# Kernel optimization log

Hardware: AMD Instinct MI355X
Metric: run time of the kernel (lower is better)

The kernel has to match this reference:

```python
import jax, jax.numpy as jnp
import numpy as np

B, L, K = 4, 1024, 48
EF, NF, NPE, NRBF, NCLS = 128, 128, 16, 16, 3
MAXREL = 32
EDGE_IN = NPE + NRBF * 25  # 416


def setup_inputs():
    key = jax.random.key(0)
    ks = jax.random.split(key, 8)
    X = jax.random.normal(ks[0], (B, L, 4, 3), jnp.float32)
    mask = jnp.ones((B, L), jnp.float32)
    R_idx = jnp.arange(B * L, dtype=jnp.int64).reshape(B, L)
    chain_labels = jax.random.randint(ks[1], (B, L), 0, 4).astype(jnp.int64)
    membrane_per_residue_labels = jax.random.randint(ks[2], (B, L), 0, NCLS).astype(jnp.int64)
    pe_w = jax.random.normal(ks[3], (2 * MAXREL + 2, NPE), jnp.float32) * 0.05
    pe_b = jax.random.normal(ks[4], (NPE,), jnp.float32) * 0.05
    edge_w = jax.random.normal(ks[5], (EDGE_IN, EF), jnp.float32) * 0.05
    ne_g = jnp.ones((EF,), jnp.float32)
    ne_b = jnp.zeros((EF,), jnp.float32)
    node_w = jax.random.normal(ks[6], (NCLS, NF), jnp.float32) * 0.05
    nn_g = jnp.ones((NF,), jnp.float32)
    nn_b = jnp.zeros((NF,), jnp.float32)
    return {"X": X, "mask": mask, "R_idx": R_idx, "chain_labels": chain_labels,
            "membrane_per_residue_labels": membrane_per_residue_labels,
            "pe_w": pe_w, "pe_b": pe_b, "edge_w": edge_w, "ne_g": ne_g, "ne_b": ne_b,
            "node_w": node_w, "nn_g": nn_g, "nn_b": nn_b}


def _rbf(D):
    mu = jnp.linspace(2.0, 22.0, NRBF)
    sigma = (22.0 - 2.0) / NRBF
    return jnp.exp(-(((D[..., None] - mu) / sigma) ** 2))


def _gather_nb(v, e_idx):
    # v: [B, L, ...] -> [B, L, K, ...] gathered along residue dim
    return jax.vmap(lambda vi, ii: vi[ii])(v, e_idx)


def _ln(x, g, b, eps=1e-5):
    mu = jnp.mean(x, -1, keepdims=True)
    var = jnp.mean((x - mu) ** 2, -1, keepdims=True)
    return (x - mu) / jnp.sqrt(var + eps) * g + b


# 24 atom-pair RBFs after the Ca-Ca (D_neighbors) one, in the original concat order
PAIRS = [("N","N"),("C","C"),("O","O"),("Cb","Cb"),("Ca","N"),("Ca","C"),("Ca","O"),
         ("Ca","Cb"),("N","C"),("N","O"),("N","Cb"),("Cb","C"),("Cb","O"),("O","C"),
         ("N","Ca"),("C","Ca"),("O","Ca"),("Cb","Ca"),("C","N"),("O","N"),("Cb","N"),
         ("C","Cb"),("O","Cb"),("C","O")]


def reference(X, mask, R_idx, chain_labels, membrane_per_residue_labels,
              pe_w, pe_b, edge_w, ne_g, ne_b, node_w, nn_g, nn_b):
    Na, Ca, Cc, Oo = X[:, :, 0], X[:, :, 1], X[:, :, 2], X[:, :, 3]
    bvec = Ca - Na
    cvec = Cc - Ca
    avec = jnp.cross(bvec, cvec)
    Cb = -0.58273431 * avec + 0.56802827 * bvec - 0.54067466 * cvec + Ca
    coords = {"N": Na, "Ca": Ca, "C": Cc, "O": Oo, "Cb": Cb}

    # masked Ca-Ca distances + kNN (single NxN pass)
    mask2 = mask[:, :, None] * mask[:, None, :]
    dX = Ca[:, :, None, :] - Ca[:, None, :, :]
    D = mask2 * jnp.sqrt(jnp.sum(dX ** 2, -1) + 1e-6)
    D_max = jnp.max(D, -1, keepdims=True)
    D_adj = D + (1.0 - mask2) * D_max
    negD, E_idx = jax.lax.top_k(-D_adj, K)
    D_neighbors = -negD  # [B, L, K]

    # gather neighbor coords once, compute the 25 RBF features on N*K pairs only
    nb = {n: _gather_nb(v, E_idx) for n, v in coords.items()}  # [B, L, K, 3]
    rbf_list = [_rbf(D_neighbors)]
    for an, bn in PAIRS:
        d = jnp.sqrt(jnp.sum((coords[an][:, :, None, :] - nb[bn]) ** 2, -1) + 1e-6)
        rbf_list.append(_rbf(d))
    RBF_all = jnp.concatenate(rbf_list, -1)  # [B, L, K, 400]

    # positional encodings on gathered offsets / chain equality
    off = R_idx[:, :, None] - _gather_nb(R_idx, E_idx)           # [B, L, K]
    E_chains = (chain_labels[:, :, None] == _gather_nb(chain_labels, E_idx)).astype(jnp.int32)
    d = jnp.clip(off + MAXREL, 0, 2 * MAXREL).astype(jnp.int32) * E_chains + (1 - E_chains) * (2 * MAXREL + 1)
    d1h = jax.nn.one_hot(d, 2 * MAXREL + 2, dtype=jnp.float32)
    E_pos = d1h @ pe_w + pe_b                                     # [B, L, K, 16]

    E = jnp.concatenate([E_pos, RBF_all], -1) @ edge_w            # [B, L, K, 128]
    E = _ln(E, ne_g, ne_b)

    C1h = jax.nn.one_hot(membrane_per_residue_labels, NCLS, dtype=jnp.float32)
    V = _ln(C1h @ node_w, nn_g, nn_b)                             # [B, L, 128]
    return V, E, E_idx
```

## Files before the change

kernel.cpp:

```cpp
#include <hip/hip_runtime.h>
#include <math.h>

#define B_ 4
#define L_ 1024
#define K_ 48
#define EF_ 128
#define NF_ 128
#define NPE_ 16
#define NRBF_ 16
#define MAXREL_ 32
#define EDGE_IN_ 416

#define V_SIZE   (B_*L_*NF_)
#define E_OFF    (V_SIZE)
#define E_SIZE   (B_*L_*K_*EF_)
#define EIDX_OFF (E_OFF + E_SIZE)

#define XH_STRIDE 232

typedef __attribute__((ext_vector_type(8))) short bf16x8;
typedef __attribute__((ext_vector_type(4))) float f32x4;
typedef __attribute__((ext_vector_type(4))) unsigned u32x4;

__device__ const int PA_[25] = {1, 0,2,3,4, 1,1,1,1, 0,0,0, 4,4, 3, 0,2,3,4, 2,3,4, 2,3, 2};
__device__ const int PB_[25] = {1, 0,2,3,4, 0,2,3,4, 2,3,4, 2,3, 2, 1,1,1,1, 0,0,0, 4,4, 3};

__device__ __forceinline__ unsigned short f2bf(float f){
    unsigned u = __float_as_uint(f);
    unsigned r = u + 0x7fffu + ((u >> 16) & 1u);
    return (unsigned short)(r >> 16);
}

__device__ __forceinline__ float pair_dist(const float* sAI, const float (*sAJ)[16], int e, int g2) {
    float dx = sAI[PA_[g2]*3+0] - sAJ[e][PB_[g2]*3+0];
    float dy = sAI[PA_[g2]*3+1] - sAJ[e][PB_[g2]*3+1];
    float dz = sAI[PA_[g2]*3+2] - sAJ[e][PB_[g2]*3+2];
    return sqrtf(dx*dx + dy*dy + dz*dz + 1e-6f);
}

__device__ __forceinline__ void rbf16(unsigned short* dst, float dist) {
    float t = 0.8f * dist - 1.6f;
    unsigned pk[8];
    #pragma unroll
    for (int rr = 0; rr < 8; ++rr) {
        float v0 = __expf(-t * t); t -= 1.06666672f;
        float v1 = __expf(-t * t); t -= 1.06666672f;
        asm("v_cvt_pk_bf16_f32 %0, %1, %2" : "=v"(pk[rr]) : "v"(v0), "v"(v1));
    }
    u32x4 w0 = {pk[0], pk[1], pk[2], pk[3]};
    u32x4 w1 = {pk[4], pk[5], pk[6], pk[7]};
    *(u32x4*)dst = w0;
    *(u32x4*)(dst + 8) = w1;
}

template<int NKS, int KB>
__device__ __forceinline__ void mfma_half(f32x4 (&acc)[3][2], const unsigned short* xh,
                                          const unsigned short* w0p, const unsigned short* w1p,
                                          int lr, int lg) {
    #pragma unroll
    for (int ks = 0; ks < NKS; ++ks) {
        int k0 = ks * 32;
        bf16x8 a0, a1, a2, wb0, wb1;
        wb0 = *(const bf16x8*)(w0p + KB + k0);
        wb1 = *(const bf16x8*)(w1p + KB + k0);
        a0 = *(const bf16x8*)&xh[(lr)      * XH_STRIDE + k0 + lg*8];
        a1 = *(const bf16x8*)&xh[(16 + lr) * XH_STRIDE + k0 + lg*8];
        a2 = *(const bf16x8*)&xh[(32 + lr) * XH_STRIDE + k0 + lg*8];
        acc[0][0] = __builtin_amdgcn_mfma_f32_16x16x32_bf16(a0, wb0, acc[0][0], 0, 0, 0);
        acc[0][1] = __builtin_amdgcn_mfma_f32_16x16x32_bf16(a0, wb1, acc[0][1], 0, 0, 0);
        acc[1][0] = __builtin_amdgcn_mfma_f32_16x16x32_bf16(a1, wb0, acc[1][0], 0, 0, 0);
        acc[1][1] = __builtin_amdgcn_mfma_f32_16x16x32_bf16(a1, wb1, acc[1][1], 0, 0, 0);
        acc[2][0] = __builtin_amdgcn_mfma_f32_16x16x32_bf16(a2, wb0, acc[2][0], 0, 0, 0);
        acc[2][1] = __builtin_amdgcn_mfma_f32_16x16x32_bf16(a2, wb1, acc[2][1], 0, 0, 0);
    }
}

__global__ __launch_bounds__(256) void wprep_kernel(const float* __restrict__ w,
                                                    unsigned short* __restrict__ wt)
{
    int idx = blockIdx.x * 256 + threadIdx.x;
    if (idx >= EDGE_IN_ * EF_) return;
    int f = idx & 127;
    int k = idx >> 7;
    wt[f * EDGE_IN_ + k] = f2bf(w[k * EF_ + f]);
}

__global__ __launch_bounds__(128) void v_kernel(const int* __restrict__ labels,
                                                const float* __restrict__ node_w,
                                                const float* __restrict__ g,
                                                const float* __restrict__ bb,
                                                float* __restrict__ out)
{
    int gi = blockIdx.x;
    int f  = threadIdx.x;
    int lbl = labels[gi];
    float v = node_w[lbl*NF_ + f];

    __shared__ float red[2];
    __shared__ float red2[2];
    float s = v;
    #pragma unroll
    for (int m = 1; m < 64; m <<= 1) s += __shfl_xor(s, m, 64);
    if ((f & 63) == 0) red[f >> 6] = s;
    __syncthreads();
    float mu = (red[0] + red[1]) * (1.0f / NF_);
    float d = v - mu;
    float s2 = d * d;
    #pragma unroll
    for (int m = 1; m < 64; m <<= 1) s2 += __shfl_xor(s2, m, 64);
    if ((f & 63) == 0) red2[f >> 6] = s2;
    __syncthreads();
    float var = (red2[0] + red2[1]) * (1.0f / NF_);
    out[gi*NF_ + f] = d * rsqrtf(var + 1e-5f) * g[f] + bb[f];
}

__global__ __launch_bounds__(256, 6) void fused_kernel(const float* __restrict__ X,
                                                   const float* __restrict__ mask,
                                                   const int* __restrict__ Ridx,
                                                   const int* __restrict__ chains,
                                                   const float* __restrict__ pe_w,
                                                   const float* __restrict__ pe_b,
                                                   const unsigned short* __restrict__ wt,
                                                   const float* __restrict__ ne_g,
                                                   const float* __restrict__ ne_b,
                                                   float* __restrict__ out)
{
    __shared__ __align__(16) unsigned char sBuf[K_ * XH_STRIDE * 2];
    __shared__ float sAI[16];
    __shared__ float sAJ[K_][16];
    __shared__ int   sJ[K_];
    __shared__ int   sDpos[K_];
    __shared__ float wmax[4];
    __shared__ unsigned wsum[4];
    __shared__ int sSelBin;
    __shared__ unsigned sSelLo, sSelCnt, sCnt, sCnt2;
    __shared__ unsigned long long sTkey;

    unsigned* hist32 = (unsigned*)sBuf;
    unsigned short* xh = (unsigned short*)sBuf;
    unsigned long long* cand = (unsigned long long*)(sBuf + 16384);
    float* stats  = (float*)(sBuf + 16384);
    float* stats2 = (float*)(sBuf + 17152);

    int tid = threadIdx.x;
    int gi  = blockIdx.x;
    int b   = gi >> 10;
    int i   = gi & (L_ - 1);

    const float* Xb = X + ((size_t)(b << 10)) * 12;
    const float* mb = mask + (b << 10);
    float cx, cy, cz, mi;
    {
        const float* xi = Xb + (size_t)i * 12 + 3;
        cx = xi[0]; cy = xi[1]; cz = xi[2];
        mi = mb[i];
    }
    if (tid == 0) { sCnt = 0; sCnt2 = 0; }

    float dist4[4], m2r[4];
    float lmax = 0.0f;
    #pragma unroll
    for (int q = 0; q < 4; ++q) {
        int j = tid + q * 256;
        const float* xj = Xb + (size_t)j * 12 + 3;
        float dx = cx - xj[0];
        float dy = cy - xj[1];
        float dz = cz - xj[2];
        float dist = sqrtf(dx*dx + dy*dy + dz*dz + 1e-6f);
        float m2 = mi * mb[j];
        dist4[q] = dist; m2r[q] = m2;
        lmax = fmaxf(lmax, m2 * dist);
    }
    #pragma unroll
    for (int m = 1; m < 64; m <<= 1) lmax = fmaxf(lmax, __shfl_xor(lmax, m, 64));
    if ((tid & 63) == 0) wmax[tid >> 6] = lmax;
    __syncthreads();
    float Dmax = fmaxf(fmaxf(wmax[0], wmax[1]), fmaxf(wmax[2], wmax[3]));

    unsigned long long key[4];
    #pragma unroll
    for (int q = 0; q < 4; ++q) {
        int j = tid + q * 256;
        float Dadj = m2r[q] * dist4[q] + (1.0f - m2r[q]) * Dmax;
        key[q] = (((unsigned long long)__float_as_uint(Dadj)) << 32) | (unsigned)j;
    }

    for (int k = tid; k < 4096; k += 256) hist32[k] = 0;
    __syncthreads();
    #pragma unroll
    for (int q = 0; q < 4; ++q)
        atomicAdd(&hist32[(unsigned)(key[q] >> 51) & 0xFFFu], 1u);
    __syncthreads();

    u32x4 h4[4];
    #pragma unroll
    for (int k = 0; k < 4; ++k) h4[k] = *(u32x4*)&hist32[tid*16 + k*4];
    unsigned loc[16], tot = 0;
    #pragma unroll
    for (int k = 0; k < 16; ++k) { tot += h4[k>>2][k&3]; loc[k] = tot; }
    unsigned ws = tot;
    #pragma unroll
    for (int m = 1; m < 64; m <<= 1) {
        unsigned o = __shfl_up(ws, m, 64);
        if ((tid & 63) >= m) ws += o;
    }
    if ((tid & 63) == 63) wsum[tid >> 6] = ws;
    __syncthreads();
    unsigned base = ws - tot;
    for (int w = 0; w < (tid >> 6); ++w) base += wsum[w];
    unsigned lo_t = base;
    #pragma unroll
    for (int k = 0; k < 16; ++k) {
        unsigned hi_t = base + loc[k];
        if (47u >= lo_t && 47u < hi_t) { sSelBin = tid*16 + k; sSelLo = lo_t; sSelCnt = hi_t - lo_t; }
        lo_t = hi_t;
    }
    __syncthreads();
    unsigned bsel = (unsigned)sSelBin, lo = sSelLo, c = sSelCnt;
    unsigned long long T;

    if (c == 1) {
        #pragma unroll
        for (int q = 0; q < 4; ++q)
            if (((unsigned)(key[q] >> 51) & 0xFFFu) == bsel) sTkey = key[q];
        __syncthreads();
        T = sTkey;
    } else if (c <= 64) {
        #pragma unroll
        for (int q = 0; q < 4; ++q)
            if (((unsigned)(key[q] >> 51) & 0xFFFu) == bsel) {
                unsigned pos = atomicAdd(&sCnt, 1u);
                cand[pos] = key[q];
            }
        __syncthreads();
        if (tid < 64) {
            unsigned long long k64 = (tid < (int)c) ? cand[tid] : 0xffffffffffffffffULL;
            #pragma unroll
            for (unsigned kk = 2; kk <= 64; kk <<= 1) {
                #pragma unroll
                for (unsigned jj = kk >> 1; jj > 0; jj >>= 1) {
                    unsigned long long o = __shfl_xor(k64, jj, 64);
                    bool lower = (tid & jj) == 0;
                    bool asc   = (tid & kk) == 0;
                    unsigned long long mn = (k64 < o) ? k64 : o;
                    unsigned long long mx = (k64 < o) ? o : k64;
                    k64 = (lower == asc) ? mn : mx;
                }
            }
            if (tid == (int)(47u - lo)) sTkey = k64;
        }
        __syncthreads();
        T = sTkey;
    } else {
        bool act[4] = {true, true, true, true};
        unsigned r = K_ - 1;
        T = 0;
        const int shifts[6] = {56, 48, 40, 32, 8, 0};
        #pragma unroll 1
        for (int p = 0; p < 6; ++p) {
            int sh = shifts[p];
            hist32[tid] = 0;
            __syncthreads();
            #pragma unroll
            for (int q = 0; q < 4; ++q)
                if (act[q]) atomicAdd(&hist32[(unsigned)((key[q] >> sh) & 255ULL)], 1u);
            __syncthreads();
            if (tid < 64) {
                unsigned b0 = hist32[tid*4+0], b1 = hist32[tid*4+1], b2 = hist32[tid*4+2], b3 = hist32[tid*4+3];
                unsigned s0 = b0, s1 = s0 + b1, s2 = s1 + b2, s3 = s2 + b3;
                unsigned s = s3;
                #pragma unroll
                for (int m = 1; m < 64; m <<= 1) {
                    unsigned o = __shfl_up(s, m, 64);
                    if (tid >= m) s += o;
                }
                unsigned bse = s - s3;
                hist32[tid*4+0] = bse + s0;
                hist32[tid*4+1] = bse + s1;
                hist32[tid*4+2] = bse + s2;
                hist32[tid*4+3] = bse + s3;
            }
            __syncthreads();
            unsigned lo2 = (tid == 0) ? 0u : hist32[tid - 1];
            unsigned hi2 = hist32[tid];
            if (r >= lo2 && r < hi2) { sSelBin = tid; sSelLo = lo2; }
            __syncthreads();
            int bs2 = sSelBin;
            r -= sSelLo;
            T |= ((unsigned long long)(unsigned)bs2) << sh;
            #pragma unroll
            for (int q = 0; q < 4; ++q)
                act[q] = act[q] && ((unsigned)((key[q] >> sh) & 255ULL) == (unsigned)bs2);
            __syncthreads();
        }
    }

    #pragma unroll
    for (int q = 0; q < 4; ++q)
        if (key[q] <= T) {
            unsigned pos = atomicAdd(&sCnt2, 1u);
            cand[pos] = key[q];
        }
    __syncthreads();

    if (tid < 64) {
        unsigned long long k64 = (tid < K_) ? cand[tid] : 0xffffffffffffffffULL;
        #pragma unroll
        for (unsigned kk = 2; kk <= 64; kk <<= 1) {
            #pragma unroll
            for (unsigned jj = kk >> 1; jj > 0; jj >>= 1) {
                unsigned long long o = __shfl_xor(k64, jj, 64);
                bool lower = (tid & jj) == 0;
                bool asc   = (tid & kk) == 0;
                unsigned long long mn = (k64 < o) ? k64 : o;
                unsigned long long mx = (k64 < o) ? o : k64;
                k64 = (lower == asc) ? mn : mx;
            }
        }
        if (tid < K_) {
            int j = (int)(unsigned)(k64 & 0xffffffffULL);
            sJ[tid] = j;
            out[EIDX_OFF + (size_t)gi * K_ + tid] = (float)j;
        }
    }
    __syncthreads();

    if (tid < K_ + 1) {
        int rr = (tid < K_) ? sJ[tid] : i;
        const float* xr = X + ((size_t)((b << 10) + rr)) * 12;
        float n0=xr[0],  n1=xr[1],  n2=xr[2];
        float a0=xr[3],  a1=xr[4],  a2=xr[5];
        float c0=xr[6],  c1=xr[7],  c2=xr[8];
        float o0=xr[9],  o1=xr[10], o2=xr[11];
        float bx=a0-n0, by=a1-n1, bz=a2-n2;
        float vx=c0-a0, vy=c1-a1, vz=c2-a2;
        float ax = by*vz - bz*vy;
        float ay = bz*vx - bx*vz;
        float az = bx*vy - by*vx;
        float cb0 = -0.58273431f*ax + 0.56802827f*bx - 0.54067466f*vx + a0;
        float cb1 = -0.58273431f*ay + 0.56802827f*by - 0.54067466f*vy + a1;
        float cb2 = -0.58273431f*az + 0.56802827f*bz - 0.54067466f*vz + a2;
        float* dst = (tid < K_) ? &sAJ[tid][0] : &sAI[0];
        dst[0]=n0;  dst[1]=n1;  dst[2]=n2;
        dst[3]=a0;  dst[4]=a1;  dst[5]=a2;
        dst[6]=c0;  dst[7]=c1;  dst[8]=c2;
        dst[9]=o0;  dst[10]=o1; dst[11]=o2;
        dst[12]=cb0; dst[13]=cb1; dst[14]=cb2;
    }
    if (tid >= 64 && tid < 64 + K_) {
        int e = tid - 64;
        int j = sJ[e];
        int off  = Ridx[gi] - Ridx[(b << 10) + j];
        int same = (chains[gi] == chains[(b << 10) + j]);
        int dcl = off + MAXREL_;
        dcl = dcl < 0 ? 0 : (dcl > 2*MAXREL_ ? 2*MAXREL_ : dcl);
        sDpos[e] = same ? dcl : (2*MAXREL_ + 1);
    }
    __syncthreads();

    const int wv = tid >> 6;
    const int ln = tid & 63;
    const int lr = ln & 15;
    const int lg = ln >> 4;

    f32x4 acc[3][2];
    #pragma unroll
    for (int rf = 0; rf < 3; ++rf)
        #pragma unroll
        for (int cf = 0; cf < 2; ++cf)
            acc[rf][cf] = (f32x4){0.0f, 0.0f, 0.0f, 0.0f};

    const unsigned short* wbase0 = wt + (size_t)(wv*32 + lr) * EDGE_IN_ + lg*8;
    const unsigned short* wbase1 = wt + (size_t)(wv*32 + 16 + lr) * EDGE_IN_ + lg*8;

    #pragma unroll
    for (int p = 0; p < 2; ++p) {
        int idx = tid + p * 256;
        if (idx < 384) {
            int e = idx >> 3, cc = (idx & 7) * 2;
            int dp = sDpos[e];
            float v0 = pe_w[dp*NPE_ + cc]     + pe_b[cc];
            float v1 = pe_w[dp*NPE_ + cc + 1] + pe_b[cc + 1];
            unsigned pk;
            asm("v_cvt_pk_bf16_f32 %0, %1, %2" : "=v"(pk) : "v"(v0), "v"(v1));
            *(unsigned*)&xh[e * XH_STRIDE + cc] = pk;
        }
    }
    #pragma unroll
    for (int p = 0; p < 3; ++p) {
        int idx = tid + p * 256;
        if (idx < 624) {
            int e = idx / 13, g = idx - e * 13;
            rbf16(&xh[e * XH_STRIDE + NPE_ + g * 16], pair_dist(sAI, sAJ, e, g));
        }
    }
    __syncthreads();
    mfma_half<7, 0>(acc, xh, wbase0, wbase1, lr, lg);
    __syncthreads();
    #pragma unroll
    for (int p = 0; p < 3; ++p) {
        int idx = tid + p * 256;
        if (idx < 576) {
            int e = idx / 12, g = 13 + (idx - e * 12);
            rbf16(&xh[e * XH_STRIDE + (g - 13) * 16], pair_dist(sAI, sAJ, e, g));
        }
    }
    __syncthreads();
    mfma_half<6, 224>(acc, xh, wbase0, wbase1, lr, lg);
    __syncthreads();

    #pragma unroll
    for (int rf = 0; rf < 3; ++rf)
        #pragma unroll
        for (int r4 = 0; r4 < 4; ++r4) {
            float v0 = acc[rf][0][r4], v1 = acc[rf][1][r4];
            float s  = v0 + v1;
            float s2 = v0*v0 + v1*v1;
            #pragma unroll
            for (int m = 1; m < 16; m <<= 1) {
                s  += __shfl_xor(s,  m, 64);
                s2 += __shfl_xor(s2, m, 64);
            }
            if (lr == 0) {
                int row = rf*16 + lg*4 + r4;
                stats [wv*K_ + row] = s;
                stats2[wv*K_ + row] = s2;
            }
        }
    __syncthreads();

    int colg = wv*32 + lr;
    float gv0 = ne_g[colg],      bv0 = ne_b[colg];
    float gv1 = ne_g[colg + 16], bv1 = ne_b[colg + 16];

    #pragma unroll
    for (int rf = 0; rf < 3; ++rf)
        #pragma unroll
        for (int r4 = 0; r4 < 4; ++r4) {
            int row = rf*16 + lg*4 + r4;
            float sum = stats [row] + stats [K_ + row] + stats [2*K_ + row] + stats [3*K_ + row];
            float sq  = stats2[row] + stats2[K_ + row] + stats2[2*K_ + row] + stats2[3*K_ + row];
            float mu   = sum * (1.0f / 128.0f);
            float var  = sq * (1.0f / 128.0f) - mu * mu;
            float rstd = rsqrtf(var + 1e-5f);
            float* dst = out + E_OFF + (size_t)(gi * K_ + row) * EF_ + colg;
            __builtin_nontemporal_store((acc[rf][0][r4] - mu) * rstd * gv0 + bv0, dst);
            __builtin_nontemporal_store((acc[rf][1][r4] - mu) * rstd * gv1 + bv1, dst + 16);
        }
}

extern "C" void kernel_launch(void* const* d_in, const int* in_sizes, int n_in,
                              void* d_out, int out_size, void* d_ws, size_t ws_size,
                              hipStream_t stream)
{
    const float* X      = (const float*)d_in[0];
    const float* mask   = (const float*)d_in[1];
    const int*   Ridx   = (const int*)d_in[2];
    const int*   chains = (const int*)d_in[3];
    const int*   memb   = (const int*)d_in[4];
    const float* pe_w   = (const float*)d_in[5];
    const float* pe_b   = (const float*)d_in[6];
    const float* edge_w = (const float*)d_in[7];
    const float* ne_g   = (const float*)d_in[8];
    const float* ne_b   = (const float*)d_in[9];
    const float* node_w = (const float*)d_in[10];
    const float* nn_g   = (const float*)d_in[11];
    const float* nn_b   = (const float*)d_in[12];
    float* out = (float*)d_out;

    unsigned short* wt = (unsigned short*)d_ws;

    wprep_kernel<<<(EDGE_IN_*EF_ + 255)/256, 256, 0, stream>>>(edge_w, wt);
    v_kernel<<<B_*L_, 128, 0, stream>>>(memb, node_w, nn_g, nn_b, out);
    fused_kernel<<<B_*L_, 256, 0, stream>>>(X, mask, Ridx, chains, pe_w, pe_b,
                                            wt, ne_g, ne_b, out);
}
```

Baseline: 88.29 us.

## Tile edge GEMM by 16-neighbor row blocks to shrink LDS and raise occupancy

```diff
diff --git a/kernel.cpp b/kernel.cpp
--- a/kernel.cpp
+++ b/kernel.cpp
@@ -16,7 +16,7 @@
 #define E_SIZE   (B_*L_*K_*EF_)
 #define EIDX_OFF (E_OFF + E_SIZE)
 
-#define XH_STRIDE 232
+#define XT_STRIDE 424
 
 typedef __attribute__((ext_vector_type(8))) short bf16x8;
 typedef __attribute__((ext_vector_type(4))) float f32x4;
@@ -53,25 +53,17 @@
     *(u32x4*)(dst + 8) = w1;
 }
 
-template<int NKS, int KB>
-__device__ __forceinline__ void mfma_half(f32x4 (&acc)[3][2], const unsigned short* xh,
+__device__ __forceinline__ void mfma_tile(f32x4 &accA, f32x4 &accB, const unsigned short* xh,
                                           const unsigned short* w0p, const unsigned short* w1p,
                                           int lr, int lg) {
     #pragma unroll
-    for (int ks = 0; ks < NKS; ++ks) {
+    for (int ks = 0; ks < 13; ++ks) {
         int k0 = ks * 32;
-        bf16x8 a0, a1, a2, wb0, wb1;
-        wb0 = *(const bf16x8*)(w0p + KB + k0);
-        wb1 = *(const bf16x8*)(w1p + KB + k0);
-        a0 = *(const bf16x8*)&xh[(lr)      * XH_STRIDE + k0 + lg*8];
-        a1 = *(const bf16x8*)&xh[(16 + lr) * XH_STRIDE + k0 + lg*8];
-        a2 = *(const bf16x8*)&xh[(32 + lr) * XH_STRIDE + k0 + lg*8];
-        acc[0][0] = __builtin_amdgcn_mfma_f32_16x16x32_bf16(a0, wb0, acc[0][0], 0, 0, 0);
-        acc[0][1] = __builtin_amdgcn_mfma_f32_16x16x32_bf16(a0, wb1, acc[0][1], 0, 0, 0);
-        acc[1][0] = __builtin_amdgcn_mfma_f32_16x16x32_bf16(a1, wb0, acc[1][0], 0, 0, 0);
-        acc[1][1] = __builtin_amdgcn_mfma_f32_16x16x32_bf16(a1, wb1, acc[1][1], 0, 0, 0);
-        acc[2][0] = __builtin_amdgcn_mfma_f32_16x16x32_bf16(a2, wb0, acc[2][0], 0, 0, 0);
-        acc[2][1] = __builtin_amdgcn_mfma_f32_16x16x32_bf16(a2, wb1, acc[2][1], 0, 0, 0);
+        bf16x8 a0  = *(const bf16x8*)&xh[lr * XT_STRIDE + k0 + lg*8];
+        bf16x8 wb0 = *(const bf16x8*)(w0p + k0);
+        bf16x8 wb1 = *(const bf16x8*)(w1p + k0);
+        accA = __builtin_amdgcn_mfma_f32_16x16x32_bf16(a0, wb0, accA, 0, 0, 0);
+        accB = __builtin_amdgcn_mfma_f32_16x16x32_bf16(a0, wb1, accB, 0, 0, 0);
     }
 }
 
@@ -114,7 +106,7 @@
     out[gi*NF_ + f] = d * rsqrtf(var + 1e-5f) * g[f] + bb[f];
 }
 
-__global__ __launch_bounds__(256, 6) void fused_kernel(const float* __restrict__ X,
+__global__ __launch_bounds__(256, 8) void fused_kernel(const float* __restrict__ X,
                                                    const float* __restrict__ mask,
                                                    const int* __restrict__ Ridx,
                                                    const int* __restrict__ chains,
@@ -125,11 +117,13 @@
                                                    const float* __restrict__ ne_b,
                                                    float* __restrict__ out)
 {
-    __shared__ __align__(16) unsigned char sBuf[K_ * XH_STRIDE * 2];
+    __shared__ __align__(16) unsigned char sBuf[16 * XT_STRIDE * 2];
     __shared__ float sAI[16];
     __shared__ float sAJ[K_][16];
     __shared__ int   sJ[K_];
     __shared__ int   sDpos[K_];
+    __shared__ float stats [4 * K_];
+    __shared__ float stats2[4 * K_];
     __shared__ float wmax[4];
     __shared__ unsigned wsum[4];
     __shared__ int sSelBin;
@@ -138,9 +132,7 @@
 
     unsigned* hist32 = (unsigned*)sBuf;
     unsigned short* xh = (unsigned short*)sBuf;
-    unsigned long long* cand = (unsigned long long*)(sBuf + 16384);
-    float* stats  = (float*)(sBuf + 16384);
-    float* stats2 = (float*)(sBuf + 17152);
+    unsigned long long* cand = (unsigned long long*)(sBuf + 8192);
 
     int tid = threadIdx.x;
     int gi  = blockIdx.x;
@@ -185,19 +177,24 @@
         key[q] = (((unsigned long long)__float_as_uint(Dadj)) << 32) | (unsigned)j;
     }
 
-    for (int k = tid; k < 4096; k += 256) hist32[k] = 0;
-    __syncthreads();
-    #pragma unroll
-    for (int q = 0; q < 4; ++q)
-        atomicAdd(&hist32[(unsigned)(key[q] >> 51) & 0xFFFu], 1u);
-    __syncthreads();
-
-    u32x4 h4[4];
-    #pragma unroll
-    for (int k = 0; k < 4; ++k) h4[k] = *(u32x4*)&hist32[tid*16 + k*4];
+    for (int k = tid; k < 2048; k += 256) hist32[k] = 0;
+    __syncthreads();
+    #pragma unroll
+    for (int q = 0; q < 4; ++q) {
+        unsigned bin = (unsigned)(key[q] >> 51) & 0xFFFu;
+        atomicAdd(&hist32[bin >> 1], 1u << ((bin & 1u) << 4));
+    }
+    __syncthreads();
+
+    u32x4 hw0 = *(u32x4*)&hist32[tid*8];
+    u32x4 hw1 = *(u32x4*)&hist32[tid*8 + 4];
     unsigned loc[16], tot = 0;
     #pragma unroll
-    for (int k = 0; k < 16; ++k) { tot += h4[k>>2][k&3]; loc[k] = tot; }
+    for (int k = 0; k < 16; ++k) {
+        unsigned w = (k < 8) ? hw0[k >> 1] : hw1[(k - 8) >> 1];
+        unsigned cnt = (k & 1) ? (w >> 16) : (w & 0xFFFFu);
+        tot += cnt; loc[k] = tot;
+    }
     unsigned ws = tot;
     #pragma unroll
     for (int m = 1; m < 64; m <<= 1) {
@@ -365,55 +362,44 @@
 
     f32x4 acc[3][2];
     #pragma unroll
-    for (int rf = 0; rf < 3; ++rf)
+    for (int t = 0; t < 3; ++t)
         #pragma unroll
         for (int cf = 0; cf < 2; ++cf)
-            acc[rf][cf] = (f32x4){0.0f, 0.0f, 0.0f, 0.0f};
+            acc[t][cf] = (f32x4){0.0f, 0.0f, 0.0f, 0.0f};
 
     const unsigned short* wbase0 = wt + (size_t)(wv*32 + lr) * EDGE_IN_ + lg*8;
     const unsigned short* wbase1 = wt + (size_t)(wv*32 + 16 + lr) * EDGE_IN_ + lg*8;
 
     #pragma unroll
-    for (int p = 0; p < 2; ++p) {
-        int idx = tid + p * 256;
-        if (idx < 384) {
-            int e = idx >> 3, cc = (idx & 7) * 2;
-            int dp = sDpos[e];
+    for (int t = 0; t < 3; ++t) {
+        if (tid < 128) {
+            int e16 = tid >> 3, cc = (tid & 7) * 2;
+            int dp = sDpos[t*16 + e16];
             float v0 = pe_w[dp*NPE_ + cc]     + pe_b[cc];
             float v1 = pe_w[dp*NPE_ + cc + 1] + pe_b[cc + 1];
             unsigned pk;
             asm("v_cvt_pk_bf16_f32 %0, %1, %2" : "=v"(pk) : "v"(v0), "v"(v1));
-            *(unsigned*)&xh[e * XH_STRIDE + cc] = pk;
-        }
-    }
-    #pragma unroll
-    for (int p = 0; p < 3; ++p) {
-        int idx = tid + p * 256;
-        if (idx < 624) {
-            int e = idx / 13, g = idx - e * 13;
-            rbf16(&xh[e * XH_STRIDE + NPE_ + g * 16], pair_dist(sAI, sAJ, e, g));
-        }
-    }
-    __syncthreads();
-    mfma_half<7, 0>(acc, xh, wbase0, wbase1, lr, lg);
-    __syncthreads();
-    #pragma unroll
-    for (int p = 0; p < 3; ++p) {
-        int idx = tid + p * 256;
-        if (idx < 576) {
-            int e = idx / 12, g = 13 + (idx - e * 12);
-            rbf16(&xh[e * XH_STRIDE + (g - 13) * 16], pair_dist(sAI, sAJ, e, g));
-        }
-    }
-    __syncthreads();
-    mfma_half<6, 224>(acc, xh, wbase0, wbase1, lr, lg);
-    __syncthreads();
-
-    #pragma unroll
-    for (int rf = 0; rf < 3; ++rf)
+            *(unsigned*)&xh[e16 * XT_STRIDE + cc] = pk;
+        }
+        #pragma unroll
+        for (int p = 0; p < 2; ++p) {
+            int idx = tid + p * 256;
+            if (idx < 400) {
+                int e16 = idx / 25, g = idx - e16 * 25;
+                rbf16(&xh[e16 * XT_STRIDE + NPE_ + g * 16],
+                      pair_dist(sAI, sAJ, t*16 + e16, g));
+            }
+        }
+        __syncthreads();
+        mfma_tile(acc[t][0], acc[t][1], xh, wbase0, wbase1, lr, lg);
+        if (t < 2) __syncthreads();
+    }
+
+    #pragma unroll
+    for (int t = 0; t < 3; ++t)
         #pragma unroll
         for (int r4 = 0; r4 < 4; ++r4) {
-            float v0 = acc[rf][0][r4], v1 = acc[rf][1][r4];
+            float v0 = acc[t][0][r4], v1 = acc[t][1][r4];
             float s  = v0 + v1;
             float s2 = v0*v0 + v1*v1;
             #pragma unroll
@@ -422,7 +408,7 @@
                 s2 += __shfl_xor(s2, m, 64);
             }
             if (lr == 0) {
-                int row = rf*16 + lg*4 + r4;
+                int row = t*16 + lg*4 + r4;
                 stats [wv*K_ + row] = s;
                 stats2[wv*K_ + row] = s2;
             }
@@ -434,18 +420,18 @@
     float gv1 = ne_g[colg + 16], bv1 = ne_b[colg + 16];
 
     #pragma unroll
-    for (int rf = 0; rf < 3; ++rf)
+    for (int t = 0; t < 3; ++t)
         #pragma unroll
         for (int r4 = 0; r4 < 4; ++r4) {
-            int row = rf*16 + lg*4 + r4;
+            int row = t*16 + lg*4 + r4;
             float sum = stats [row] + stats [K_ + row] + stats [2*K_ + row] + stats [3*K_ + row];
             float sq  = stats2[row] + stats2[K_ + row] + stats2[2*K_ + row] + stats2[3*K_ + row];
             float mu   = sum * (1.0f / 128.0f);
             float var  = sq * (1.0f / 128.0f) - mu * mu;
             float rstd = rsqrtf(var + 1e-5f);
             float* dst = out + E_OFF + (size_t)(gi * K_ + row) * EF_ + colg;
-            __builtin_nontemporal_store((acc[rf][0][r4] - mu) * rstd * gv0 + bv0, dst);
-            __builtin_nontemporal_store((acc[rf][1][r4] - mu) * rstd * gv1 + bv1, dst + 16);
+            __builtin_nontemporal_store((acc[t][0][r4] - mu) * rstd * gv0 + bv0, dst);
+            __builtin_nontemporal_store((acc[t][1][r4] - mu) * rstd * gv1 + bv1, dst + 16);
         }
 }
 
```

After: 139.1 us. 57.5% more time.
